# Performance work log

Measured on AMD Instinct MI355X. Metric: run time of the kernel, lower is better.

The kernel has to match this reference:

```python
import jax, jax.numpy as jnp
import numpy as np

B, T, H, S = 2, 2048, 16, 64
EMB = H * S  # 1024


def layer_norm(x, g, b, eps=1e-5):
    mu = jnp.mean(x, axis=-1, keepdims=True)
    var = jnp.var(x, axis=-1, keepdims=True)
    return (x - mu) * jax.lax.rsqrt(var + eps) * g + b


def setup_inputs() -> dict:
    key = jax.random.key(0)
    ks = jax.random.split(key, 12)
    sc = 0.02
    return {
        "x": jax.random.normal(ks[0], (B, T, EMB), dtype=jnp.float32),
        "Wkqv": jax.random.normal(ks[1], (S, 3 * S), dtype=jnp.float32) * sc,
        "Wproj": jax.random.normal(ks[2], (EMB, EMB), dtype=jnp.float32) * sc,
        "g1": jnp.ones((EMB,), jnp.float32),
        "b1": jnp.zeros((EMB,), jnp.float32),
        "W1": jax.random.normal(ks[3], (EMB, 4 * EMB), dtype=jnp.float32) * sc,
        "bff1": jnp.zeros((4 * EMB,), jnp.float32),
        "W2": jax.random.normal(ks[4], (4 * EMB, EMB), dtype=jnp.float32) * sc,
        "bff2": jnp.zeros((EMB,), jnp.float32),
        "g2": jnp.ones((EMB,), jnp.float32),
        "b2": jnp.zeros((EMB,), jnp.float32),
    }


def reference(x, Wkqv, Wproj, g1, b1, W1, bff1, W2, bff2, g2, b2):
    Bb, Tt, _ = x.shape
    xh = x.reshape(Bb, Tt, H, S)                     # [B,T,H,S]
    kqv = jnp.einsum('bths,sd->bthd', xh, Wkqv)      # [B,T,H,3S], shared per-head weight
    k, q, v = jnp.split(kqv, 3, axis=-1)             # note order: k, q, v
    scores = jnp.einsum('bihk,bjhk->bijh', q, k) / jnp.sqrt(jnp.float32(S))
    att = jax.nn.softmax(scores, axis=2)             # softmax over key dim j
    res = jnp.einsum('btih,bihs->bths', att, v).reshape(Bb, Tt, EMB)
    mha = res @ Wproj                                # Linear(emb, emb, bias=False)
    x = layer_norm(x + mha, g1, b1)
    h = jax.nn.gelu(x @ W1 + bff1, approximate=False)
    ff = h @ W2 + bff2
    return layer_norm(x + ff, g2, b2)
```

## Files before the change

### kernel.cpp

```cpp
#include <hip/hip_runtime.h>
#include <hip/hip_bf16.h>
#include <math.h>

#define B_ 2
#define T_ 2048
#define H_ 16
#define S_ 64
#define EMB 1024
#define FF 4096
#define BT (B_*T_)
#define ROWS (B_*T_*H_)

typedef __attribute__((ext_vector_type(8))) short s16x8;
typedef __attribute__((ext_vector_type(4))) float f32x4;

struct P4 { unsigned short* p[4]; };

__device__ __forceinline__ unsigned short f2b(float f) {
    return __builtin_bit_cast(unsigned short, __float2bfloat16(f));
}
__device__ __forceinline__ float b2f(short u) {
    return __builtin_bit_cast(float, ((unsigned int)(unsigned short)u) << 16);
}

__device__ __forceinline__ void gl_lds16(const void* g, void* l) {
    __builtin_amdgcn_global_load_lds(
        (const __attribute__((address_space(1))) void*)g,
        (__attribute__((address_space(3))) void*)l, 16, 0, 0);
}

__device__ __forceinline__ f32x4 mfma16(s16x8 a, s16x8 b, f32x4 c) {
    return __builtin_amdgcn_mfma_f32_16x16x32_bf16(a, b, c, 0, 0, 0);
}

#define WAIT_VM8 0x0F78
#define WAIT_VM0 0x0F70

__global__ __launch_bounds__(256) void kqv_kernel(const float* __restrict__ x,
        const unsigned short* __restrict__ Wqt, unsigned short* __restrict__ K,
        unsigned short* __restrict__ Q, unsigned short* __restrict__ V) {
    const int tid = threadIdx.x;
    const int w = tid >> 6, lane = tid & 63;
    const int l15 = lane & 15, quad = lane >> 4;
    const long r0 = (long)blockIdx.x * 128 + w * 32;

    s16x8 af[2][2];
    #pragma unroll
    for (int mt = 0; mt < 2; ++mt)
        #pragma unroll
        for (int ks = 0; ks < 2; ++ks) {
            const float* xp = x + (r0 + mt*16 + l15) * 64 + ks*32 + quad*8;
            const float4 v0 = *(const float4*)xp;
            const float4 v1 = *(const float4*)(xp + 4);
            s16x8 a;
            a[0] = (short)f2b(v0.x); a[1] = (short)f2b(v0.y);
            a[2] = (short)f2b(v0.z); a[3] = (short)f2b(v0.w);
            a[4] = (short)f2b(v1.x); a[5] = (short)f2b(v1.y);
            a[6] = (short)f2b(v1.z); a[7] = (short)f2b(v1.w);
            af[mt][ks] = a;
        }

    #pragma unroll
    for (int nt = 0; nt < 12; ++nt) {
        const s16x8 b0 = *(const s16x8*)&Wqt[(nt*16 + l15)*64 + quad*8];
        const s16x8 b1 = *(const s16x8*)&Wqt[(nt*16 + l15)*64 + 32 + quad*8];
        f32x4 acc[2] = {};
        #pragma unroll
        for (int mt = 0; mt < 2; ++mt) {
            acc[mt] = mfma16(af[mt][0], b0, acc[mt]);
            acc[mt] = mfma16(af[mt][1], b1, acc[mt]);
        }
        unsigned short* dst = (nt < 4) ? K : (nt < 8) ? Q : V;
        const int c0 = (nt & 3) * 16 + l15;
        #pragma unroll
        for (int mt = 0; mt < 2; ++mt)
            #pragma unroll
            for (int r = 0; r < 4; ++r)
                dst[(r0 + mt*16 + quad*4 + r) * 64 + c0] = f2b(acc[mt][r]);
    }
}

__global__ __launch_bounds__(256) void vt_kernel(const unsigned short* __restrict__ V,
        unsigned short* __restrict__ VT) {
    __shared__ unsigned short Ts[64][72];
    const int tid = threadIdx.x;
    const int tt = blockIdx.x, bh = blockIdx.y;
    const int b = bh >> 4, h = bh & 15;
    const long vbase = ((long)b * (T_*H_) + h) * 64;
    #pragma unroll
    for (int i = 0; i < 2; ++i) {
        const int id = i * 256 + tid;
        const int tr = id >> 3, dc = (id & 7) * 8;
        const s16x8 v = *(const s16x8*)&V[vbase + (long)(tt*64 + tr)*1024 + dc];
        *(s16x8*)&Ts[tr][dc] = v;
    }
    __syncthreads();
    #pragma unroll
    for (int i = 0; i < 2; ++i) {
        const int id = i * 256 + tid;
        const int d = id >> 3, tc = (id & 7) * 8;
        s16x8 o;
        #pragma unroll
        for (int j = 0; j < 8; ++j) o[j] = (short)Ts[tc + j][d];
        *(s16x8*)&VT[((long)bh*64 + d)*2048 + tt*64 + tc] = o;
    }
}

__global__ __launch_bounds__(64, 2) void attn_kernel(const unsigned short* __restrict__ Q,
        const unsigned short* __restrict__ K, const unsigned short* __restrict__ VT,
        unsigned short* __restrict__ res) {
    __shared__ __align__(16) unsigned short Kbuf[2][2][32*32];
    __shared__ __align__(16) unsigned short Vbuf[2][64*32];
    __shared__ __align__(16) unsigned short Ps[32*36];
    const int lane = threadIdx.x;
    const int l15 = lane & 15, quad = lane >> 4;
    const int bid = blockIdx.x;
    const int qt = bid & 63, bh = bid >> 6;
    const int b = bh >> 4, h = bh & 15;
    const long base = ((long)b * (T_*H_) + h) * 64;
    const unsigned short* Qp = Q + base;
    const unsigned short* Kp = K + base;
    const unsigned short* Vp = VT + (long)bh * 64 * 2048;
    const int q0 = qt * 32;

    s16x8 qf[2][2];
    #pragma unroll
    for (int qq = 0; qq < 2; ++qq)
        #pragma unroll
        for (int ks = 0; ks < 2; ++ks) {
            const s16x8 raw = *(const s16x8*)&Qp[(long)(q0 + qq*16 + l15)*1024 + ks*32 + quad*8];
            s16x8 q;
            #pragma unroll
            for (int j = 0; j < 8; ++j) q[j] = (short)f2b(b2f(raw[j]) * 0.125f);
            qf[qq][ks] = q;
        }

    s16x8 onef;
    #pragma unroll
    for (int j = 0; j < 8; ++j) onef[j] = (short)0x3F80;

    f32x4 oacc[2][4] = {};
    f32x4 lacc[2] = {};

    const int j16 = lane >> 2;
    const int c8  = (lane & 3) * 8;

    auto stage = [&](int bufi, int kt) {
        const unsigned short* kg = Kp + (long)(kt*32) * 1024;
        char* kl = (char*)&Kbuf[bufi][0][0];
        gl_lds16(kg + (long)j16*1024 + c8,           kl +    0 + lane*16);
        gl_lds16(kg + (long)(j16+16)*1024 + c8,      kl + 1024 + lane*16);
        gl_lds16(kg + (long)j16*1024 + 32 + c8,      kl + 2048 + lane*16);
        gl_lds16(kg + (long)(j16+16)*1024 + 32 + c8, kl + 3072 + lane*16);
        const unsigned short* vg = Vp + kt*32 + c8;
        char* vl = (char*)&Vbuf[bufi][0];
        gl_lds16(vg + (long)(j16     )*2048, vl +    0 + lane*16);
        gl_lds16(vg + (long)(j16 + 16)*2048, vl + 1024 + lane*16);
        gl_lds16(vg + (long)(j16 + 32)*2048, vl + 2048 + lane*16);
        gl_lds16(vg + (long)(j16 + 48)*2048, vl + 3072 + lane*16);
    };

    auto compute = [&](int bufi) {
        f32x4 sT[2][2] = {};
        #pragma unroll
        for (int ks = 0; ks < 2; ++ks)
            #pragma unroll
            for (int jt = 0; jt < 2; ++jt) {
                const s16x8 kf = *(const s16x8*)&Kbuf[bufi][ks][(jt*16 + l15)*32 + quad*8];
                sT[jt][0] = mfma16(kf, qf[0][ks], sT[jt][0]);
                sT[jt][1] = mfma16(kf, qf[1][ks], sT[jt][1]);
            }
        #pragma unroll
        for (int jt = 0; jt < 2; ++jt)
            #pragma unroll
            for (int qq = 0; qq < 2; ++qq) {
                uint2 pk;
                pk.x = (unsigned int)f2b(__expf(sT[jt][qq][0]))
                     | ((unsigned int)f2b(__expf(sT[jt][qq][1])) << 16);
                pk.y = (unsigned int)f2b(__expf(sT[jt][qq][2]))
                     | ((unsigned int)f2b(__expf(sT[jt][qq][3])) << 16);
                *(uint2*)&Ps[(qq*16 + l15)*36 + jt*16 + quad*4] = pk;
            }
        s16x8 pf[2];
        #pragma unroll
        for (int qq = 0; qq < 2; ++qq) {
            pf[qq] = *(const s16x8*)&Ps[(qq*16 + l15)*36 + quad*8];
            lacc[qq] = mfma16(pf[qq], onef, lacc[qq]);
        }
        #pragma unroll
        for (int nt = 0; nt < 4; ++nt) {
            const s16x8 vf = *(const s16x8*)&Vbuf[bufi][(nt*16 + l15)*32 + quad*8];
            oacc[0][nt] = mfma16(pf[0], vf, oacc[0][nt]);
            oacc[1][nt] = mfma16(pf[1], vf, oacc[1][nt]);
        }
    };

    stage(0, 0);
    for (int kt = 0; kt < 63; ++kt) {
        stage((kt + 1) & 1, kt + 1);
        __builtin_amdgcn_s_waitcnt(WAIT_VM8);
        __builtin_amdgcn_sched_barrier(0);
        compute(kt & 1);
    }
    __builtin_amdgcn_s_waitcnt(WAIT_VM0);
    __builtin_amdgcn_sched_barrier(0);
    compute(1);

    #pragma unroll
    for (int qq = 0; qq < 2; ++qq)
        #pragma unroll
        for (int r = 0; r < 4; ++r) {
            const float inv = 1.f / lacc[qq][r];
            const int t = q0 + qq*16 + quad*4 + r;
            #pragma unroll
            for (int nt = 0; nt < 4; ++nt)
                res[((long)(b*T_ + t))*EMB + h*64 + nt*16 + l15] =
                    f2b(oacc[qq][nt][r] * inv);
        }
}

__global__ __launch_bounds__(256) void gemm_gelu(const unsigned short* __restrict__ A,
        const unsigned short* __restrict__ Bt, const float* __restrict__ bias,
        unsigned short* __restrict__ C, int M, int N, int Kd) {
    __shared__ __align__(16) unsigned short As[128 * 32];
    __shared__ __align__(16) unsigned short Bs[128 * 32];
    const int tid = threadIdx.x;
    const int w = tid >> 6, lane = tid & 63;
    const int l15 = lane & 15, quad = lane >> 4;
    const int wm = w >> 1, wn = w & 1;
    const int bn = blockIdx.x, bm = blockIdx.y;
    const int sr = lane >> 2, skq = lane & 3;
    f32x4 acc[4][4] = {};
    const long arow = (long)(bm*128 + w*32 + sr);
    const long brow = (long)(bn*128 + w*32 + sr);

    for (int kt = 0; kt < Kd; kt += 32) {
        gl_lds16(A  + (arow     )*Kd + kt + skq*8, (char*)As + (w*32     )*64 + lane*16);
        gl_lds16(A  + (arow + 16)*Kd + kt + skq*8, (char*)As + (w*32 + 16)*64 + lane*16);
        gl_lds16(Bt + (brow     )*Kd + kt + skq*8, (char*)Bs + (w*32     )*64 + lane*16);
        gl_lds16(Bt + (brow + 16)*Kd + kt + skq*8, (char*)Bs + (w*32 + 16)*64 + lane*16);
        __syncthreads();
        s16x8 af[4], bf[4];
        #pragma unroll
        for (int mt = 0; mt < 4; ++mt)
            af[mt] = *(const s16x8*)&As[(wm*64 + mt*16 + l15)*32 + quad*8];
        #pragma unroll
        for (int nt = 0; nt < 4; ++nt)
            bf[nt] = *(const s16x8*)&Bs[(wn*64 + nt*16 + l15)*32 + quad*8];
        #pragma unroll
        for (int mt = 0; mt < 4; ++mt)
            #pragma unroll
            for (int nt = 0; nt < 4; ++nt)
                acc[mt][nt] = mfma16(af[mt], bf[nt], acc[mt][nt]);
        __syncthreads();
    }

    #pragma unroll
    for (int mt = 0; mt < 4; ++mt) {
        const int row0 = bm*128 + wm*64 + mt*16 + quad*4;
        #pragma unroll
        for (int nt = 0; nt < 4; ++nt) {
            const int col = bn*128 + wn*64 + nt*16 + l15;
            const float bv = bias[col];
            #pragma unroll
            for (int r = 0; r < 4; ++r) {
                float v = acc[mt][nt][r] + bv;
                v = 0.5f * v * (1.f + erff(v * 0.70710678118654752440f));
                C[(long)(row0 + r)*N + col] = f2b(v);
            }
        }
    }
}

__global__ __launch_bounds__(256) void gemm_splitk(const unsigned short* __restrict__ A,
        const unsigned short* __restrict__ Bt, P4 parts, int M, int N, int Kd, int Ks) {
    __shared__ __align__(16) unsigned short As[128 * 32];
    __shared__ __align__(16) unsigned short Bs[128 * 32];
    const int tid = threadIdx.x;
    const int w = tid >> 6, lane = tid & 63;
    const int l15 = lane & 15, quad = lane >> 4;
    const int wm = w >> 1, wn = w & 1;
    const int bn = blockIdx.x, bm = blockIdx.y, s = blockIdx.z;
    const int sr = lane >> 2, skq = lane & 3;
    f32x4 acc[4][4] = {};
    const long arow = (long)(bm*128 + w*32 + sr);
    const long brow = (long)(bn*128 + w*32 + sr);
    const int k0 = s * Ks;

    for (int kt = k0; kt < k0 + Ks; kt += 32) {
        gl_lds16(A  + (arow     )*Kd + kt + skq*8, (char*)As + (w*32     )*64 + lane*16);
        gl_lds16(A  + (arow + 16)*Kd + kt + skq*8, (char*)As + (w*32 + 16)*64 + lane*16);
        gl_lds16(Bt + (brow     )*Kd + kt + skq*8, (char*)Bs + (w*32     )*64 + lane*16);
        gl_lds16(Bt + (brow + 16)*Kd + kt + skq*8, (char*)Bs + (w*32 + 16)*64 + lane*16);
        __syncthreads();
        s16x8 af[4], bf[4];
        #pragma unroll
        for (int mt = 0; mt < 4; ++mt)
            af[mt] = *(const s16x8*)&As[(wm*64 + mt*16 + l15)*32 + quad*8];
        #pragma unroll
        for (int nt = 0; nt < 4; ++nt)
            bf[nt] = *(const s16x8*)&Bs[(wn*64 + nt*16 + l15)*32 + quad*8];
        #pragma unroll
        for (int mt = 0; mt < 4; ++mt)
            #pragma unroll
            for (int nt = 0; nt < 4; ++nt)
                acc[mt][nt] = mfma16(af[mt], bf[nt], acc[mt][nt]);
        __syncthreads();
    }

    unsigned short* Cp = parts.p[s];
    #pragma unroll
    for (int mt = 0; mt < 4; ++mt) {
        const int row0 = bm*128 + wm*64 + mt*16 + quad*4;
        #pragma unroll
        for (int nt = 0; nt < 4; ++nt) {
            const int col = bn*128 + wn*64 + nt*16 + l15;
            #pragma unroll
            for (int r = 0; r < 4; ++r)
                Cp[(long)(row0 + r)*N + col] = f2b(acc[mt][nt][r]);
        }
    }
}

template <int P, int XBF>
__global__ __launch_bounds__(256) void ln_kernel(const void* __restrict__ xa,
        P4 parts, const float* __restrict__ addb, const float* __restrict__ g,
        const float* __restrict__ bia, float* __restrict__ out,
        unsigned short* __restrict__ outb) {
    const int row = blockIdx.x;
    const int tid = threadIdx.x;
    float4 v;
    if (XBF) {
        const ushort4 u = ((const ushort4*)xa)[(long)row * (EMB/4) + tid];
        v.x = b2f((short)u.x); v.y = b2f((short)u.y);
        v.z = b2f((short)u.z); v.w = b2f((short)u.w);
    } else {
        v = ((const float4*)xa)[(long)row * (EMB/4) + tid];
    }
    #pragma unroll
    for (int p = 0; p < P; ++p) {
        const ushort4 u = ((const ushort4*)(parts.p[p] + (long)row * EMB))[tid];
        v.x += b2f((short)u.x); v.y += b2f((short)u.y);
        v.z += b2f((short)u.z); v.w += b2f((short)u.w);
    }
    if (addb) {
        const float4 ab = ((const float4*)addb)[tid];
        v.x += ab.x; v.y += ab.y; v.z += ab.z; v.w += ab.w;
    }
    float s = v.x + v.y + v.z + v.w;
    float ss = v.x * v.x + v.y * v.y + v.z * v.z + v.w * v.w;
    #pragma unroll
    for (int off = 32; off > 0; off >>= 1) {
        s += __shfl_down(s, off, 64);
        ss += __shfl_down(ss, off, 64);
    }
    __shared__ float ls[4], lss[4];
    __shared__ float mean_s, rstd_s;
    const int wid = tid >> 6, lane = tid & 63;
    if (lane == 0) { ls[wid] = s; lss[wid] = ss; }
    __syncthreads();
    if (tid == 0) {
        const float S0 = ls[0] + ls[1] + ls[2] + ls[3];
        const float S2 = lss[0] + lss[1] + lss[2] + lss[3];
        const float mean = S0 * (1.f / EMB);
        const float var = S2 * (1.f / EMB) - mean * mean;
        mean_s = mean;
        rstd_s = rsqrtf(var + 1e-5f);
    }
    __syncthreads();
    const float mean = mean_s, rstd = rstd_s;
    const float4 gg = ((const float4*)g)[tid];
    const float4 bb = ((const float4*)bia)[tid];
    float4 o;
    o.x = (v.x - mean) * rstd * gg.x + bb.x;
    o.y = (v.y - mean) * rstd * gg.y + bb.y;
    o.z = (v.z - mean) * rstd * gg.z + bb.z;
    o.w = (v.w - mean) * rstd * gg.w + bb.w;
    if (out) ((float4*)(out + (long)row * EMB))[tid] = o;
    if (outb) {
        unsigned short* ob = outb + (long)row * EMB + tid * 4;
        ob[0] = f2b(o.x); ob[1] = f2b(o.y); ob[2] = f2b(o.z); ob[3] = f2b(o.w);
    }
}

__global__ __launch_bounds__(256) void transp_all(const float* __restrict__ Wp,
        const float* __restrict__ W1, const float* __restrict__ W2,
        const float* __restrict__ Wq, unsigned short* __restrict__ Wpt,
        unsigned short* __restrict__ W1t, unsigned short* __restrict__ W2t,
        unsigned short* __restrict__ Wqt) {
    int id = blockIdx.x;
    const float* W; unsigned short* Wt; int Kd, N, ntx;
    if (id < 1024)      {            W = Wp; Wt = Wpt; Kd = 1024; N = 1024; ntx = 32; }
    else if (id < 5120) { id -= 1024; W = W1; Wt = W1t; Kd = 1024; N = 4096; ntx = 128; }
    else if (id < 9216) { id -= 5120; W = W2; Wt = W2t; Kd = 4096; N = 1024; ntx = 32; }
    else                { id -= 9216; W = Wq; Wt = Wqt; Kd = 64;   N = 192;  ntx = 6;  }
    __shared__ float Ts[32][33];
    const int tid = threadIdx.x;
    const int n0 = (id % ntx) * 32, k0 = (id / ntx) * 32;
    const int r = tid >> 3, c4 = (tid & 7) * 4;
    const float4 v = *(const float4*)&W[(long)(k0 + r) * N + n0 + c4];
    Ts[r][c4] = v.x; Ts[r][c4 + 1] = v.y; Ts[r][c4 + 2] = v.z; Ts[r][c4 + 3] = v.w;
    __syncthreads();
    #pragma unroll
    for (int i = 0; i < 4; ++i)
        Wt[(long)(n0 + r) * Kd + k0 + c4 + i] = f2b(Ts[c4 + i][r]);
}

extern "C" void kernel_launch(void* const* d_in, const int* in_sizes, int n_in,
                              void* d_out, int out_size, void* d_ws, size_t ws_size,
                              hipStream_t stream) {
    (void)in_sizes; (void)n_in; (void)out_size;
    const float* x     = (const float*)d_in[0];
    const float* Wkqv  = (const float*)d_in[1];
    const float* Wproj = (const float*)d_in[2];
    const float* g1    = (const float*)d_in[3];
    const float* b1    = (const float*)d_in[4];
    const float* W1    = (const float*)d_in[5];
    const float* bff1  = (const float*)d_in[6];
    const float* W2    = (const float*)d_in[7];
    const float* bff2  = (const float*)d_in[8];
    const float* g2    = (const float*)d_in[9];
    const float* b2    = (const float*)d_in[10];
    float* out = (float*)d_out;
    char* ws = (char*)d_ws;

    const size_t MB = 1u << 20;
    unsigned short* Qb   = (unsigned short*)(ws + 0 * MB);
    unsigned short* Kb   = (unsigned short*)(ws + 8 * MB);
    unsigned short* Vb   = (unsigned short*)(ws + 16 * MB);
    unsigned short* resb = (unsigned short*)(ws + 24 * MB);
    unsigned short* hb   = (unsigned short*)(ws + 8 * MB);
    unsigned short* VTb  = (unsigned short*)(ws + 40 * MB);
    unsigned short* mp0  = (unsigned short*)(ws + 40 * MB);
    unsigned short* mp1  = (unsigned short*)(ws + 48 * MB);
    unsigned short* x1b  = Qb;
    unsigned short* Wpt  = (unsigned short*)(ws + 72 * MB);
    unsigned short* W1t  = (unsigned short*)(ws + 74 * MB);
    unsigned short* W2t  = (unsigned short*)(ws + 82 * MB);
    unsigned short* Wqt  = (unsigned short*)(ws + 90 * MB);
    unsigned short* fp2  = (unsigned short*)(ws + 91 * MB);
    unsigned short* fp3  = (unsigned short*)(ws + 99 * MB);
    const bool big = ws_size >= 108 * MB;

    transp_all<<<dim3(9228), 256, 0, stream>>>(Wproj, W1, W2, Wkqv, Wpt, W1t, W2t, Wqt);

    kqv_kernel<<<dim3(ROWS/128), 256, 0, stream>>>(x, Wqt, Kb, Qb, Vb);
    vt_kernel<<<dim3(T_/64, B_*H_), 256, 0, stream>>>(Vb, VTb);
    attn_kernel<<<dim3(2048), 64, 0, stream>>>(Qb, Kb, VTb, resb);
    P4 mp; mp.p[0] = mp0; mp.p[1] = mp1; mp.p[2] = nullptr; mp.p[3] = nullptr;
    gemm_splitk<<<dim3(EMB/128, BT/128, 2), 256, 0, stream>>>(resb, Wpt, mp, BT, EMB, EMB, EMB/2);
    ln_kernel<2, 0><<<dim3(BT), 256, 0, stream>>>(x, mp, nullptr, g1, b1, nullptr, x1b);
    gemm_gelu<<<dim3(FF/128, BT/128), 256, 0, stream>>>(x1b, W1t, bff1, hb, BT, FF, EMB);
    if (big) {
        P4 fp; fp.p[0] = mp0; fp.p[1] = mp1; fp.p[2] = fp2; fp.p[3] = fp3;
        gemm_splitk<<<dim3(EMB/128, BT/128, 4), 256, 0, stream>>>(hb, W2t, fp, BT, EMB, FF, FF/4);
        ln_kernel<4, 1><<<dim3(BT), 256, 0, stream>>>(x1b, fp, bff2, g2, b2, out, nullptr);
    } else {
        P4 fp; fp.p[0] = mp0; fp.p[1] = mp1; fp.p[2] = nullptr; fp.p[3] = nullptr;
        gemm_splitk<<<dim3(EMB/128, BT/128, 2), 256, 0, stream>>>(hb, W2t, fp, BT, EMB, FF, FF/2);
        ln_kernel<2, 1><<<dim3(BT), 256, 0, stream>>>(x1b, fp, bff2, g2, b2, out, nullptr);
    }
}
```

Before: 364.9 us.

## Double-buffer LDS tiles in GELU and split-K GEMMs to overlap loads

Both bf16 MFMA GEMM kernels now keep two shared-memory buffers for the A and B tiles. The global-to-LDS copy for the next K-step is issued before computing on the current one, and one barrier per iteration replaces two. The goal is to hide global load latency behind MFMA work. It doubles LDS use per block, which may lower occupancy, and correctness depends on gl_lds16 completion being covered by the single __syncthreads.

```diff
diff --git a/kernel.cpp b/kernel.cpp
--- a/kernel.cpp
+++ b/kernel.cpp
@@ -222,8 +222,8 @@
 __global__ __launch_bounds__(256) void gemm_gelu(const unsigned short* __restrict__ A,
         const unsigned short* __restrict__ Bt, const float* __restrict__ bias,
         unsigned short* __restrict__ C, int M, int N, int Kd) {
-    __shared__ __align__(16) unsigned short As[128 * 32];
-    __shared__ __align__(16) unsigned short Bs[128 * 32];
+    __shared__ __align__(16) unsigned short As[2][128 * 32];
+    __shared__ __align__(16) unsigned short Bs[2][128 * 32];
     const int tid = threadIdx.x;
     const int w = tid >> 6, lane = tid & 63;
     const int l15 = lane & 15, quad = lane >> 4;
@@ -234,25 +234,35 @@
     const long arow = (long)(bm*128 + w*32 + sr);
     const long brow = (long)(bn*128 + w*32 + sr);
 
-    for (int kt = 0; kt < Kd; kt += 32) {
-        gl_lds16(A  + (arow     )*Kd + kt + skq*8, (char*)As + (w*32     )*64 + lane*16);
-        gl_lds16(A  + (arow + 16)*Kd + kt + skq*8, (char*)As + (w*32 + 16)*64 + lane*16);
-        gl_lds16(Bt + (brow     )*Kd + kt + skq*8, (char*)Bs + (w*32     )*64 + lane*16);
-        gl_lds16(Bt + (brow + 16)*Kd + kt + skq*8, (char*)Bs + (w*32 + 16)*64 + lane*16);
-        __syncthreads();
+    auto stage = [&](int bi, int kt) {
+        char* as = (char*)&As[bi][0];
+        char* bs = (char*)&Bs[bi][0];
+        gl_lds16(A  + (arow     )*Kd + kt + skq*8, as + (w*32     )*64 + lane*16);
+        gl_lds16(A  + (arow + 16)*Kd + kt + skq*8, as + (w*32 + 16)*64 + lane*16);
+        gl_lds16(Bt + (brow     )*Kd + kt + skq*8, bs + (w*32     )*64 + lane*16);
+        gl_lds16(Bt + (brow + 16)*Kd + kt + skq*8, bs + (w*32 + 16)*64 + lane*16);
+    };
+
+    const int NT = Kd >> 5;
+    stage(0, 0);
+    __syncthreads();
+    int bi = 0;
+    for (int t = 0; t < NT; ++t) {
+        if (t + 1 < NT) stage(bi ^ 1, (t + 1) * 32);
         s16x8 af[4], bf[4];
         #pragma unroll
         for (int mt = 0; mt < 4; ++mt)
-            af[mt] = *(const s16x8*)&As[(wm*64 + mt*16 + l15)*32 + quad*8];
+            af[mt] = *(const s16x8*)&As[bi][(wm*64 + mt*16 + l15)*32 + quad*8];
         #pragma unroll
         for (int nt = 0; nt < 4; ++nt)
-            bf[nt] = *(const s16x8*)&Bs[(wn*64 + nt*16 + l15)*32 + quad*8];
+            bf[nt] = *(const s16x8*)&Bs[bi][(wn*64 + nt*16 + l15)*32 + quad*8];
         #pragma unroll
         for (int mt = 0; mt < 4; ++mt)
             #pragma unroll
             for (int nt = 0; nt < 4; ++nt)
                 acc[mt][nt] = mfma16(af[mt], bf[nt], acc[mt][nt]);
         __syncthreads();
+        bi ^= 1;
     }
 
     #pragma unroll
@@ -274,8 +284,8 @@
 
 __global__ __launch_bounds__(256) void gemm_splitk(const unsigned short* __restrict__ A,
         const unsigned short* __restrict__ Bt, P4 parts, int M, int N, int Kd, int Ks) {
-    __shared__ __align__(16) unsigned short As[128 * 32];
-    __shared__ __align__(16) unsigned short Bs[128 * 32];
+    __shared__ __align__(16) unsigned short As[2][128 * 32];
+    __shared__ __align__(16) unsigned short Bs[2][128 * 32];
     const int tid = threadIdx.x;
     const int w = tid >> 6, lane = tid & 63;
     const int l15 = lane & 15, quad = lane >> 4;
@@ -287,25 +297,35 @@
     const long brow = (long)(bn*128 + w*32 + sr);
     const int k0 = s * Ks;
 
-    for (int kt = k0; kt < k0 + Ks; kt += 32) {
-        gl_lds16(A  + (arow     )*Kd + kt + skq*8, (char*)As + (w*32     )*64 + lane*16);
-        gl_lds16(A  + (arow + 16)*Kd + kt + skq*8, (char*)As + (w*32 + 16)*64 + lane*16);
-        gl_lds16(Bt + (brow     )*Kd + kt + skq*8, (char*)Bs + (w*32     )*64 + lane*16);
-        gl_lds16(Bt + (brow + 16)*Kd + kt + skq*8, (char*)Bs + (w*32 + 16)*64 + lane*16);
-        __syncthreads();
+    auto stage = [&](int bi, int kt) {
+        char* as = (char*)&As[bi][0];
+        char* bs = (char*)&Bs[bi][0];
+        gl_lds16(A  + (arow     )*Kd + kt + skq*8, as + (w*32     )*64 + lane*16);
+        gl_lds16(A  + (arow + 16)*Kd + kt + skq*8, as + (w*32 + 16)*64 + lane*16);
+        gl_lds16(Bt + (brow     )*Kd + kt + skq*8, bs + (w*32     )*64 + lane*16);
+        gl_lds16(Bt + (brow + 16)*Kd + kt + skq*8, bs + (w*32 + 16)*64 + lane*16);
+    };
+
+    const int NT = Ks >> 5;
+    stage(0, k0);
+    __syncthreads();
+    int bi = 0;
+    for (int t = 0; t < NT; ++t) {
+        if (t + 1 < NT) stage(bi ^ 1, k0 + (t + 1) * 32);
         s16x8 af[4], bf[4];
         #pragma unroll
         for (int mt = 0; mt < 4; ++mt)
-            af[mt] = *(const s16x8*)&As[(wm*64 + mt*16 + l15)*32 + quad*8];
+            af[mt] = *(const s16x8*)&As[bi][(wm*64 + mt*16 + l15)*32 + quad*8];
         #pragma unroll
         for (int nt = 0; nt < 4; ++nt)
-            bf[nt] = *(const s16x8*)&Bs[(wn*64 + nt*16 + l15)*32 + quad*8];
+            bf[nt] = *(const s16x8*)&Bs[bi][(wn*64 + nt*16 + l15)*32 + quad*8];
         #pragma unroll
         for (int mt = 0; mt < 4; ++mt)
             #pragma unroll
             for (int nt = 0; nt < 4; ++nt)
                 acc[mt][nt] = mfma16(af[mt], bf[nt], acc[mt][nt]);
         __syncthreads();
+        bi ^= 1;
     }
 
     unsigned short* Cp = parts.p[s];
```

Result: faster. 352.6 us (-3.4%).
